# Performance work log

Hardware: AMD Instinct MI355X
Metric: run time of the kernel (lower is better)

The kernel has to match this reference:

```python
import jax, jax.numpy as jnp
import numpy as np

N, E = 50000, 800000
F, H, M = 64, 128, 64  # feature_dim, hidden_dim, message_dim (message_dim must equal feature_dim)


def _mlp(x, W1, b1, W2, b2):
    return jnp.maximum(x @ W1 + b1, 0.0) @ W2 + b2


def setup_inputs() -> dict:
    key = jax.random.key(0)
    ks = jax.random.split(key, 20)
    p = lambda k, s: (jax.random.normal(k, s, jnp.float32) * 0.05)
    return {
        "z_h": jax.random.normal(ks[0], (N, F), jnp.float32),
        "pos_world": jax.random.normal(ks[1], (3,), jnp.float32),
        "edge_index": jax.random.randint(ks[2], (2, E), 0, N),
        "We1": p(ks[3], (2 * F + 8, H)), "be1": p(ks[4], (H,)),
        "We2": p(ks[5], (H, M)), "be2": p(ks[6], (M,)),
        "Wg1": p(ks[7], (2 * F + 8, H)), "bg1": p(ks[8], (H,)),
        "Wg2": p(ks[9], (H, 1)), "bg2": p(ks[10], (1,)),
        "Wn1": p(ks[11], (F + M, H)), "bn1": p(ks[12], (H,)),
        "Wn2": p(ks[13], (H, F)), "bn2": p(ks[14], (F,)),
        "Ww1": p(ks[15], (F + 3, H)), "bw1": p(ks[16], (H,)),
        "Ww2": p(ks[17], (H, M)), "bw2": p(ks[18], (M,)),
    }


def reference(z_h, pos_world, edge_index,
              We1, be1, We2, be2,
              Wg1, bg1, Wg2, bg2,
              Wn1, bn1, Wn2, bn2,
              Ww1, bw1, Ww2, bw2):
    src, tgt = edge_index[0], edge_index[1]
    zs = z_h[src]  # [E, F]
    zt = z_h[tgt]  # [E, F]

    # edge features: diff(3) + dist(1) + vel cross product(3) + its norm(1)
    diff = zs[:, 0:3] - zt[:, 0:3]
    dist = jnp.sum(diff * diff, axis=-1, keepdims=True)
    cross = jnp.cross(zs[:, 3:6], zt[:, 3:6])
    cross_n = jnp.linalg.norm(cross, axis=-1, keepdims=True)
    e_feat = jnp.concatenate([diff, dist, cross, cross_n], axis=-1)  # [E, 8]

    inp_edge = jnp.concatenate([zs, zt, e_feat], axis=-1)  # [E, 2F+8]
    m = _mlp(inp_edge, We1, be1, We2, be2)                 # [E, M]
    w = jax.nn.sigmoid(_mlp(inp_edge, Wg1, bg1, Wg2, bg2))  # [E, 1]

    # scatter_add weighted messages to target nodes
    m_agg_h = jax.ops.segment_sum(w * m, tgt, num_segments=N)  # [N, F] (M == F)

    # world message: sum over all nodes, broadcast back
    diff_world = z_h[:, 0:3] - pos_world
    inp_world = jnp.concatenate([z_h, diff_world], axis=-1)  # [N, F+3]
    m_h_w = _mlp(inp_world, Ww1, bw1, Ww2, bw2)              # [N, M]
    m_agg_w = jnp.sum(m_h_w, axis=0, keepdims=True)          # [1, M] -> broadcast

    m_agg_total = m_agg_h + m_agg_w
    inp_node = jnp.concatenate([z_h, m_agg_total], axis=-1)  # [N, F+M]
    delta_z_h = _mlp(inp_node, Wn1, bn1, Wn2, bn2)           # [N, F]
    return delta_z_h
```

## Files before the change

### kernel.cpp

```cpp
#include <hip/hip_runtime.h>
#include <math.h>

#define NN 50000
#define NE 800000
#define EBLOCKS (NE / 64)
#define WBLOCKS ((NN + 63) / 64)

typedef float     f32x4  __attribute__((ext_vector_type(4)));
typedef __bf16    bf16x8 __attribute__((ext_vector_type(8)));
typedef _Float16  f16x2  __attribute__((ext_vector_type(2)));
typedef _Float16  f16x8  __attribute__((ext_vector_type(8)));

#define WE1F_OFF 0
#define WE2F_OFF 5120
#define WN1F_OFF 6144
#define WN2F_OFF 8192
#define WW1F_OFF 9216
#define WW2F_OFF 10752
#define NCHUNKS  11776


__device__ inline bf16x8 pack8(float4 a, float4 b) {
    bf16x8 r;
    r[0] = (__bf16)a.x; r[1] = (__bf16)a.y; r[2] = (__bf16)a.z; r[3] = (__bf16)a.w;
    r[4] = (__bf16)b.x; r[5] = (__bf16)b.y; r[6] = (__bf16)b.z; r[7] = (__bf16)b.w;
    return r;
}

__device__ inline void pk_atomic_add_f16(void* addr, f16x2 v) {
#if __has_builtin(__builtin_amdgcn_global_atomic_fadd_v2f16)
    __builtin_amdgcn_global_atomic_fadd_v2f16((f16x2*)addr, v);
#else
    asm volatile("global_atomic_pk_add_f16 %0, %1, off"
                 :: "v"(addr), "v"(v) : "memory");
#endif
}

__global__ __launch_bounds__(256) void pack_weights(
    const float* __restrict__ We1, const float* __restrict__ Wg1,
    const float* __restrict__ We2, const float* __restrict__ Wn1,
    const float* __restrict__ Wn2, const float* __restrict__ Ww1,
    const float* __restrict__ Ww2, bf16x8* __restrict__ wsF)
{
    int c = blockIdx.x * 256 + threadIdx.x;
    if (c >= NCHUNKS) return;
    const int lane = c & 63, l16 = lane & 15, row8 = ((lane >> 4) & 3) * 8;
    bf16x8 p;
    if (c < WE2F_OFF) {
        int ct = (c >> 6) & 15, kc = c >> 10;
        int col = ct * 16 + l16;
        const float* src = (col < 128) ? (We1 + col) : (Wg1 + (col - 128));
#pragma unroll
        for (int i = 0; i < 8; i++) {
            int r = kc * 32 + row8 + i;
            p[i] = (__bf16)((r < 136) ? src[(size_t)r * 128] : 0.f);
        }
    } else if (c < WN1F_OFF) {
        int cc = c - WE2F_OFF; int ct = (cc >> 6) & 3, kc = cc >> 8;
        int col = ct * 16 + l16;
#pragma unroll
        for (int i = 0; i < 8; i++)
            p[i] = (__bf16)We2[(size_t)(kc * 32 + row8 + i) * 64 + col];
    } else if (c < WN2F_OFF) {
        int cc = c - WN1F_OFF; int ct = (cc >> 6) & 7, kc = cc >> 9;
        int col = ct * 16 + l16;
#pragma unroll
        for (int i = 0; i < 8; i++)
            p[i] = (__bf16)Wn1[(size_t)(kc * 32 + row8 + i) * 128 + col];
    } else if (c < WW1F_OFF) {
        int cc = c - WN2F_OFF; int ct = (cc >> 6) & 3, kc = cc >> 8;
        int col = ct * 16 + l16;
#pragma unroll
        for (int i = 0; i < 8; i++)
            p[i] = (__bf16)Wn2[(size_t)(kc * 32 + row8 + i) * 64 + col];
    } else if (c < WW2F_OFF) {
        int cc = c - WW1F_OFF; int ct = (cc >> 6) & 7, kc = cc >> 9;
        int col = ct * 16 + l16;
#pragma unroll
        for (int i = 0; i < 8; i++) {
            int r = kc * 32 + row8 + i;
            p[i] = (__bf16)((r < 67) ? Ww1[(size_t)r * 128 + col] : 0.f);
        }
    } else {
        int cc = c - WW2F_OFF; int ct = (cc >> 6) & 3, kc = cc >> 8;
        int col = ct * 16 + l16;
#pragma unroll
        for (int i = 0; i < 8; i++)
            p[i] = (__bf16)Ww2[(size_t)(kc * 32 + row8 + i) * 64 + col];
    }
    wsF[c] = p;
}

union FusedLds {
    bf16x8 XF[1280];
    struct {
        bf16x8   HF[1024];
        _Float16 M[64 * 68];
    } s;
};

__global__ __launch_bounds__(512, 6) void fused_kernel(
    const float* __restrict__ z_h, const int* __restrict__ ei,
    const bf16x8* __restrict__ We1F, const bf16x8* __restrict__ We2F,
    const float* __restrict__ be1, const float* __restrict__ be2,
    const float* __restrict__ bg1, const float* __restrict__ Wg2,
    const float* __restrict__ bg2,
    const float* __restrict__ pos_world,
    const bf16x8* __restrict__ Ww1F, const bf16x8* __restrict__ Ww2F,
    const float* __restrict__ bw1, const float* __restrict__ bw2,
    float* __restrict__ magg_rows,
    float* __restrict__ m_agg_w)
{
    __shared__ FusedLds U;
    __shared__ int   tgt_s[64];
    __shared__ float gred[4][64];
    __shared__ float wgt[64];

    const int t = threadIdx.x;
    const int lane = t & 63, w = t >> 6;
    const int quad = lane >> 4, l16 = lane & 15;

    if (blockIdx.x >= EBLOCKS) {
        const int n0 = (blockIdx.x - EBLOCKS) * 64;
        {
            int nn = t >> 3, q = t & 7;
            int mt = nn >> 4, l16e = nn & 15;
            int node = n0 + nn; if (node >= NN) node = NN - 1;
            if (q < 4) {
                const float4* zr = (const float4*)(z_h + (long)node * 64) + q * 4;
                float4 a0 = zr[0], a1 = zr[1], a2 = zr[2], a3 = zr[3];
                int kcs = q >> 1, qa = (q & 1) * 2;
                U.XF[(kcs * 4 + mt) * 64 + qa * 16 + l16e]       = pack8(a0, a1);
                U.XF[(kcs * 4 + mt) * 64 + (qa + 1) * 16 + l16e] = pack8(a2, a3);
            } else if (q == 4) {
                float4 a0 = *(const float4*)(z_h + (long)node * 64);
                bf16x8 f;
#pragma unroll
                for (int i = 0; i < 8; i++) f[i] = (__bf16)0.f;
                f[0] = (__bf16)(a0.x - pos_world[0]);
                f[1] = (__bf16)(a0.y - pos_world[1]);
                f[2] = (__bf16)(a0.z - pos_world[2]);
                U.XF[(8 + mt) * 64 + l16e] = f;
            } else {
                bf16x8 z;
#pragma unroll
                for (int i = 0; i < 8; i++) z[i] = (__bf16)0.f;
                U.XF[(8 + mt) * 64 + (q - 4) * 16 + l16e] = z;
            }
        }
        __syncthreads();

        f32x4 acc[4];
        {
            float b = bw1[w * 16 + l16];
#pragma unroll
            for (int mt = 0; mt < 4; mt++) { f32x4 v = {b, b, b, b}; acc[mt] = v; }
        }
#pragma unroll
        for (int kc = 0; kc < 3; kc++) {
            bf16x8 bfr = Ww1F[(kc * 8 + w) * 64 + lane];
#pragma unroll
            for (int mt = 0; mt < 4; mt++)
                acc[mt] = __builtin_amdgcn_mfma_f32_16x16x32_bf16(
                    U.XF[(kc * 4 + mt) * 64 + lane], bfr, acc[mt], 0, 0, 0);
        }
        __syncthreads();

        {
            __bf16* HFp = (__bf16*)U.s.HF;
            int cw = w * 16 + l16;
            int kc2 = cw >> 5, quad2 = (cw >> 3) & 3, ii = cw & 7;
#pragma unroll
            for (int mt = 0; mt < 4; mt++)
#pragma unroll
                for (int r = 0; r < 4; r++)
                    HFp[(((kc2 * 4 + mt) * 64) + quad2 * 16 + quad * 4 + r) * 8 + ii] =
                        (__bf16)fmaxf(acc[mt][r], 0.f);
        }
        __syncthreads();

        {
            const int nt = w & 3, mh = w >> 2;
            f32x4 acc2[2];
            float b2 = bw2[nt * 16 + l16];
#pragma unroll
            for (int m = 0; m < 2; m++) { f32x4 v = {b2, b2, b2, b2}; acc2[m] = v; }
#pragma unroll
            for (int kc = 0; kc < 4; kc++) {
                bf16x8 b2f = Ww2F[(kc * 4 + nt) * 64 + lane];
#pragma unroll
                for (int m = 0; m < 2; m++)
                    acc2[m] = __builtin_amdgcn_mfma_f32_16x16x32_bf16(
                        U.s.HF[(kc * 4 + mh * 2 + m) * 64 + lane], b2f, acc2[m], 0, 0, 0);
            }
            float s = 0.f;
#pragma unroll
            for (int m = 0; m < 2; m++)
#pragma unroll
                for (int r = 0; r < 4; r++) {
                    int node = n0 + (mh * 2 + m) * 16 + quad * 4 + r;
                    s += (node < NN) ? acc2[m][r] : 0.f;
                }
            s += __shfl_xor(s, 16, 64);
            s += __shfl_xor(s, 32, 64);
            if (quad == 0) atomicAdd(m_agg_w + nt * 16 + l16, s);
        }
        return;
    }

    const int e0 = blockIdx.x * 64;

    {
        const int ee = t >> 3, q = t & 7;
        const int side = q >> 2, sub = q & 3;
        const int mt = ee >> 4, l16e = ee & 15;
        const int eg = e0 + ee;
        const int row = side ? ei[NE + eg] : ei[eg];
        if (q == 4) tgt_s[ee] = row;
        const float4* zr = (const float4*)(z_h + (long)row * 64) + sub * 4;
        float4 a0 = zr[0], a1 = zr[1], a2 = zr[2], a3 = zr[3];
        const int kcs = (sub >> 1) + side * 2, qa = (sub & 1) * 2;
        U.XF[(kcs * 4 + mt) * 64 + qa * 16 + l16e]       = pack8(a0, a1);
        U.XF[(kcs * 4 + mt) * 64 + (qa + 1) * 16 + l16e] = pack8(a2, a3);
        if (q == 0) {
            const float4* zt = (const float4*)(z_h + (long)ei[NE + eg] * 64);
            float4 t0 = zt[0], t1 = zt[1];
            float dx = a0.x - t0.x, dy = a0.y - t0.y, dz = a0.z - t0.z;
            float ax = a0.w, ay = a1.x, az = a1.y;
            float bx = t0.w, by = t1.x, bz = t1.y;
            float cx = ay * bz - az * by;
            float cy = az * bx - ax * bz;
            float cz = ax * by - ay * bx;
            bf16x8 f;
            f[0] = (__bf16)dx; f[1] = (__bf16)dy; f[2] = (__bf16)dz;
            f[3] = (__bf16)(dx * dx + dy * dy + dz * dz);
            f[4] = (__bf16)cx; f[5] = (__bf16)cy; f[6] = (__bf16)cz;
            f[7] = (__bf16)sqrtf(cx * cx + cy * cy + cz * cz);
            U.XF[(16 + mt) * 64 + l16e] = f;
        } else if (q >= 5) {
            bf16x8 z;
#pragma unroll
            for (int i = 0; i < 8; i++) z[i] = (__bf16)0.f;
            U.XF[(16 + mt) * 64 + (q - 4) * 16 + l16e] = z;
        }
    }
    __syncthreads();

    f32x4 acc[4][2];
#pragma unroll
    for (int nt = 0; nt < 2; nt++) {
        int col = (w * 2 + nt) * 16 + l16;
        float b = (col < 128) ? be1[col] : bg1[col - 128];
#pragma unroll
        for (int mt = 0; mt < 4; mt++) { f32x4 v = {b, b, b, b}; acc[mt][nt] = v; }
    }
    bf16x8 bcur0 = We1F[(w * 2) * 64 + lane];
    bf16x8 bcur1 = We1F[(w * 2 + 1) * 64 + lane];
#pragma unroll
    for (int kc = 0; kc < 5; kc++) {
        bf16x8 bnx0, bnx1;
        if (kc < 4) {
            bnx0 = We1F[((kc + 1) * 16 + w * 2) * 64 + lane];
            bnx1 = We1F[((kc + 1) * 16 + w * 2 + 1) * 64 + lane];
        }
#pragma unroll
        for (int mt = 0; mt < 4; mt++) {
            bf16x8 af = U.XF[(kc * 4 + mt) * 64 + lane];
            acc[mt][0] = __builtin_amdgcn_mfma_f32_16x16x32_bf16(af, bcur0, acc[mt][0], 0, 0, 0);
            acc[mt][1] = __builtin_amdgcn_mfma_f32_16x16x32_bf16(af, bcur1, acc[mt][1], 0, 0, 0);
        }
        bcur0 = bnx0; bcur1 = bnx1;
    }
    __syncthreads();

    if (w < 4) {
        __bf16* HFp = (__bf16*)U.s.HF;
#pragma unroll
        for (int nt = 0; nt < 2; nt++) {
            int cw = (w * 2 + nt) * 16 + l16;
            int kc2 = cw >> 5, quad2 = (cw >> 3) & 3, ii = cw & 7;
#pragma unroll
            for (int mt = 0; mt < 4; mt++)
#pragma unroll
                for (int r = 0; r < 4; r++)
                    HFp[(((kc2 * 4 + mt) * 64) + quad2 * 16 + quad * 4 + r) * 8 + ii] =
                        (__bf16)fmaxf(acc[mt][nt][r], 0.f);
        }
    } else {
        float gp[4][4];
#pragma unroll
        for (int mt = 0; mt < 4; mt++)
#pragma unroll
            for (int r = 0; r < 4; r++) gp[mt][r] = 0.f;
#pragma unroll
        for (int nt = 0; nt < 2; nt++) {
            float wg = Wg2[((w - 4) * 2 + nt) * 16 + l16];
#pragma unroll
            for (int mt = 0; mt < 4; mt++)
#pragma unroll
                for (int r = 0; r < 4; r++)
                    gp[mt][r] += fmaxf(acc[mt][nt][r], 0.f) * wg;
        }
#pragma unroll
        for (int mask = 1; mask < 16; mask <<= 1)
#pragma unroll
            for (int mt = 0; mt < 4; mt++)
#pragma unroll
                for (int r = 0; r < 4; r++)
                    gp[mt][r] += __shfl_xor(gp[mt][r], mask, 64);
        if (l16 == 0) {
#pragma unroll
            for (int mt = 0; mt < 4; mt++)
#pragma unroll
                for (int r = 0; r < 4; r++)
                    gred[(w - 4) & 3][mt * 16 + quad * 4 + r] = gp[mt][r];
        }
    }
    __syncthreads();

    if (t < 64) {
        float g = bg2[0] + gred[0][t] + gred[1][t] + gred[2][t] + gred[3][t];
        wgt[t] = 1.f / (1.f + __expf(-g));
    }

    f32x4 acc2[4];
    if (w < 4) {
        float b2 = be2[w * 16 + l16];
#pragma unroll
        for (int mt = 0; mt < 4; mt++) { f32x4 v = {b2, b2, b2, b2}; acc2[mt] = v; }
        bf16x8 c2 = We2F[w * 64 + lane];
#pragma unroll
        for (int kc = 0; kc < 4; kc++) {
            bf16x8 n2;
            if (kc < 3) n2 = We2F[((kc + 1) * 4 + w) * 64 + lane];
#pragma unroll
            for (int mt = 0; mt < 4; mt++)
                acc2[mt] = __builtin_amdgcn_mfma_f32_16x16x32_bf16(
                    U.s.HF[(kc * 4 + mt) * 64 + lane], c2, acc2[mt], 0, 0, 0);
            c2 = n2;
        }
    }
    __syncthreads();

    if (w < 4) {
#pragma unroll
        for (int mt = 0; mt < 4; mt++)
#pragma unroll
            for (int r = 0; r < 4; r++) {
                int edge = mt * 16 + quad * 4 + r;
                U.s.M[edge * 68 + w * 16 + l16] =
                    (_Float16)(acc2[mt][r] * wgt[edge]);
            }
    }
    __syncthreads();

    {
        const int p = t & 31, eb = t >> 5;
        char* base = (char*)magg_rows;
#pragma unroll
        for (int k = 0; k < 4; k++) {
            int e = eb + k * 16;
            f16x2 v = *(const f16x2*)&U.s.M[e * 68 + p * 2];
            pk_atomic_add_f16(base + (long)tgt_s[e] * 256 + p * 4, v);
        }
    }
}

__global__ __launch_bounds__(512, 4) void node_kernel(
    const float* __restrict__ z_h,
    const float* __restrict__ m_agg_w,
    const bf16x8* __restrict__ Wn1F, const bf16x8* __restrict__ Wn2F,
    const float* __restrict__ bn1, const float* __restrict__ bn2,
    float* __restrict__ outp)
{
    __shared__ union { bf16x8 XF[1024]; bf16x8 HF[1024]; } U;
    const int t = threadIdx.x;
    const int n0 = blockIdx.x * 64;
    const int lane = t & 63, w = t >> 6;
    const int quad = lane >> 4, l16 = lane & 15;

    {
        int nn = t >> 3, q = t & 7;
        int mt = nn >> 4, l16e = nn & 15;
        int node = n0 + nn; if (node >= NN) node = NN - 1;
        int half = q >> 2, sub = q & 3;
        bf16x8 c0, c1;
        if (half == 0) {
            const float4* zr = (const float4*)(z_h + (long)node * 64) + sub * 4;
            c0 = pack8(zr[0], zr[1]);
            c1 = pack8(zr[2], zr[3]);
        } else {
            const f16x8* mr = (const f16x8*)((const char*)outp + (long)node * 256) + sub * 2;
            f16x8 r0 = mr[0], r1 = mr[1];
            const float* mw = m_agg_w + sub * 16;
#pragma unroll
            for (int i = 0; i < 8; i++) {
                c0[i] = (__bf16)((float)r0[i] + mw[i]);
                c1[i] = (__bf16)((float)r1[i] + mw[i + 8]);
            }
        }
        int kcs = (sub >> 1) + half * 2, qa = (sub & 1) * 2;
        U.XF[(kcs * 4 + mt) * 64 + qa * 16 + l16e]       = c0;
        U.XF[(kcs * 4 + mt) * 64 + (qa + 1) * 16 + l16e] = c1;
    }
    __syncthreads();

    f32x4 acc[4];
    {
        float b = bn1[w * 16 + l16];
#pragma unroll
        for (int mt = 0; mt < 4; mt++) { f32x4 v = {b, b, b, b}; acc[mt] = v; }
    }
#pragma unroll
    for (int kc = 0; kc < 4; kc++) {
        bf16x8 bfr = Wn1F[(kc * 8 + w) * 64 + lane];
#pragma unroll
        for (int mt = 0; mt < 4; mt++)
            acc[mt] = __builtin_amdgcn_mfma_f32_16x16x32_bf16(
                U.XF[(kc * 4 + mt) * 64 + lane], bfr, acc[mt], 0, 0, 0);
    }
    __syncthreads();

    {
        __bf16* HFp = (__bf16*)U.HF;
        int cw = w * 16 + l16;
        int kc2 = cw >> 5, quad2 = (cw >> 3) & 3, ii = cw & 7;
#pragma unroll
        for (int mt = 0; mt < 4; mt++)
#pragma unroll
            for (int r = 0; r < 4; r++)
                HFp[(((kc2 * 4 + mt) * 64) + quad2 * 16 + quad * 4 + r) * 8 + ii] =
                    (__bf16)fmaxf(acc[mt][r], 0.f);
    }
    __syncthreads();

    {
        const int nt = w & 3, mh = w >> 2;
        f32x4 acc2[2];
        float b2 = bn2[nt * 16 + l16];
#pragma unroll
        for (int m = 0; m < 2; m++) { f32x4 v = {b2, b2, b2, b2}; acc2[m] = v; }
#pragma unroll
        for (int kc = 0; kc < 4; kc++) {
            bf16x8 b2f = Wn2F[(kc * 4 + nt) * 64 + lane];
#pragma unroll
            for (int m = 0; m < 2; m++)
                acc2[m] = __builtin_amdgcn_mfma_f32_16x16x32_bf16(
                    U.HF[(kc * 4 + mh * 2 + m) * 64 + lane], b2f, acc2[m], 0, 0, 0);
        }
#pragma unroll
        for (int m = 0; m < 2; m++)
#pragma unroll
            for (int r = 0; r < 4; r++) {
                int node = n0 + (mh * 2 + m) * 16 + quad * 4 + r;
                if (node < NN)
                    outp[(long)node * 64 + nt * 16 + l16] = acc2[m][r];
            }
    }
}

extern "C" void kernel_launch(void* const* d_in, const int* in_sizes, int n_in,
                              void* d_out, int out_size, void* d_ws, size_t ws_size,
                              hipStream_t stream)
{
    const float* z_h       = (const float*)d_in[0];
    const float* pos_world = (const float*)d_in[1];
    const int*   ei        = (const int*)d_in[2];
    const float* We1 = (const float*)d_in[3];  const float* be1 = (const float*)d_in[4];
    const float* We2 = (const float*)d_in[5];  const float* be2 = (const float*)d_in[6];
    const float* Wg1 = (const float*)d_in[7];  const float* bg1 = (const float*)d_in[8];
    const float* Wg2 = (const float*)d_in[9];  const float* bg2 = (const float*)d_in[10];
    const float* Wn1 = (const float*)d_in[11]; const float* bn1 = (const float*)d_in[12];
    const float* Wn2 = (const float*)d_in[13]; const float* bn2 = (const float*)d_in[14];
    const float* Ww1 = (const float*)d_in[15]; const float* bw1 = (const float*)d_in[16];
    const float* Ww2 = (const float*)d_in[17]; const float* bw2 = (const float*)d_in[18];

    float*  outp    = (float*)d_out;
    float*  m_agg_w = (float*)d_ws;
    bf16x8* wsF     = (bf16x8*)((char*)d_ws + 256);

    hipMemsetAsync(d_out, 0, (size_t)NN * 64 * sizeof(float), stream);
    hipMemsetAsync(d_ws, 0, 256, stream);

    pack_weights<<<(NCHUNKS + 255) / 256, 256, 0, stream>>>(
        We1, Wg1, We2, Wn1, Wn2, Ww1, Ww2, wsF);
    fused_kernel<<<EBLOCKS + WBLOCKS, 512, 0, stream>>>(
        z_h, ei, wsF + WE1F_OFF, wsF + WE2F_OFF,
        be1, be2, bg1, Wg2, bg2,
        pos_world, wsF + WW1F_OFF, wsF + WW2F_OFF, bw1, bw2,
        outp, m_agg_w);
    node_kernel<<<(NN + 63) / 64, 512, 0, stream>>>(
        z_h, m_agg_w, wsF + WN1F_OFF, wsF + WN2F_OFF, bn1, bn2, outp);
}
```

Measured before the change: 295.7 us.

## Process 128 edges per block in fused edge kernel

Doubles the edge tile from 64 to 128 edges per block, so each wave's weight fragments loaded from global memory are reused across twice as many MFMA row tiles. The gather is reorganized so each thread loads both the source and target rows for one quarter of an edge, which also removes the separate target reload used for edge features. This doubles the accumulator register and LDS footprint, and the launch bound drops from 6 to 4 blocks per CU, which may reduce occupancy and latency hiding for the gather-heavy loads. The world-message blocks share the kernel and now run with the same larger LDS allocation.

Result: no change. 296.8 us (+0.4%).

```diff
diff --git a/kernel.cpp b/kernel.cpp
--- a/kernel.cpp
+++ b/kernel.cpp
@@ -3,7 +3,8 @@
 
 #define NN 50000
 #define NE 800000
-#define EBLOCKS (NE / 64)
+#define EB 128
+#define EBLOCKS (NE / EB)
 #define WBLOCKS ((NN + 63) / 64)
 
 typedef float     f32x4  __attribute__((ext_vector_type(4)));
@@ -92,14 +93,14 @@
 }
 
 union FusedLds {
-    bf16x8 XF[1280];
+    bf16x8 XF[2560];
     struct {
-        bf16x8   HF[1024];
-        _Float16 M[64 * 68];
+        bf16x8   HF[2048];
+        _Float16 M[EB * 68];
     } s;
 };
 
-__global__ __launch_bounds__(512, 6) void fused_kernel(
+__global__ __launch_bounds__(512, 4) void fused_kernel(
     const float* __restrict__ z_h, const int* __restrict__ ei,
     const bf16x8* __restrict__ We1F, const bf16x8* __restrict__ We2F,
     const float* __restrict__ be1, const float* __restrict__ be2,
@@ -112,9 +113,9 @@
     float* __restrict__ m_agg_w)
 {
     __shared__ FusedLds U;
-    __shared__ int   tgt_s[64];
-    __shared__ float gred[4][64];
-    __shared__ float wgt[64];
+    __shared__ int   tgt_s[EB];
+    __shared__ float gred[4][EB];
+    __shared__ float wgt[EB];
 
     const int t = threadIdx.x;
     const int lane = t & 63, w = t >> 6;
@@ -208,26 +209,28 @@
         return;
     }
 
-    const int e0 = blockIdx.x * 64;
-
-    {
-        const int ee = t >> 3, q = t & 7;
-        const int side = q >> 2, sub = q & 3;
+    const int e0 = blockIdx.x * EB;
+
+    {
+        const int ee = t >> 2, sub = t & 3;
         const int mt = ee >> 4, l16e = ee & 15;
         const int eg = e0 + ee;
-        const int row = side ? ei[NE + eg] : ei[eg];
-        if (q == 4) tgt_s[ee] = row;
-        const float4* zr = (const float4*)(z_h + (long)row * 64) + sub * 4;
-        float4 a0 = zr[0], a1 = zr[1], a2 = zr[2], a3 = zr[3];
-        const int kcs = (sub >> 1) + side * 2, qa = (sub & 1) * 2;
-        U.XF[(kcs * 4 + mt) * 64 + qa * 16 + l16e]       = pack8(a0, a1);
-        U.XF[(kcs * 4 + mt) * 64 + (qa + 1) * 16 + l16e] = pack8(a2, a3);
-        if (q == 0) {
-            const float4* zt = (const float4*)(z_h + (long)ei[NE + eg] * 64);
-            float4 t0 = zt[0], t1 = zt[1];
-            float dx = a0.x - t0.x, dy = a0.y - t0.y, dz = a0.z - t0.z;
+        const int rs = ei[eg], rt = ei[NE + eg];
+        if (sub == 0) tgt_s[ee] = rt;
+        const int qa = (sub & 1) * 2;
+        const float4* zs = (const float4*)(z_h + (long)rs * 64) + sub * 4;
+        float4 a0 = zs[0], a1 = zs[1], a2 = zs[2], a3 = zs[3];
+        const float4* zt = (const float4*)(z_h + (long)rt * 64) + sub * 4;
+        float4 b0 = zt[0], b1 = zt[1], b2 = zt[2], b3 = zt[3];
+        const int kcs = (sub >> 1);
+        U.XF[(kcs * 8 + mt) * 64 + qa * 16 + l16e]             = pack8(a0, a1);
+        U.XF[(kcs * 8 + mt) * 64 + (qa + 1) * 16 + l16e]       = pack8(a2, a3);
+        U.XF[((kcs + 2) * 8 + mt) * 64 + qa * 16 + l16e]       = pack8(b0, b1);
+        U.XF[((kcs + 2) * 8 + mt) * 64 + (qa + 1) * 16 + l16e] = pack8(b2, b3);
+        if (sub == 0) {
+            float dx = a0.x - b0.x, dy = a0.y - b0.y, dz = a0.z - b0.z;
             float ax = a0.w, ay = a1.x, az = a1.y;
-            float bx = t0.w, by = t1.x, bz = t1.y;
+            float bx = b0.w, by = b1.x, bz = b1.y;
             float cx = ay * bz - az * by;
             float cy = az * bx - ax * bz;
             float cz = ax * by - ay * bx;
@@ -236,23 +239,23 @@
             f[3] = (__bf16)(dx * dx + dy * dy + dz * dz);
             f[4] = (__bf16)cx; f[5] = (__bf16)cy; f[6] = (__bf16)cz;
             f[7] = (__bf16)sqrtf(cx * cx + cy * cy + cz * cz);
-            U.XF[(16 + mt) * 64 + l16e] = f;
-        } else if (q >= 5) {
+            U.XF[(32 + mt) * 64 + l16e] = f;
+        } else {
             bf16x8 z;
 #pragma unroll
             for (int i = 0; i < 8; i++) z[i] = (__bf16)0.f;
-            U.XF[(16 + mt) * 64 + (q - 4) * 16 + l16e] = z;
-        }
-    }
-    __syncthreads();
-
-    f32x4 acc[4][2];
+            U.XF[(32 + mt) * 64 + sub * 16 + l16e] = z;
+        }
+    }
+    __syncthreads();
+
+    f32x4 acc[8][2];
 #pragma unroll
     for (int nt = 0; nt < 2; nt++) {
         int col = (w * 2 + nt) * 16 + l16;
         float b = (col < 128) ? be1[col] : bg1[col - 128];
 #pragma unroll
-        for (int mt = 0; mt < 4; mt++) { f32x4 v = {b, b, b, b}; acc[mt][nt] = v; }
+        for (int mt = 0; mt < 8; mt++) { f32x4 v = {b, b, b, b}; acc[mt][nt] = v; }
     }
     bf16x8 bcur0 = We1F[(w * 2) * 64 + lane];
     bf16x8 bcur1 = We1F[(w * 2 + 1) * 64 + lane];
@@ -264,8 +267,8 @@
             bnx1 = We1F[((kc + 1) * 16 + w * 2 + 1) * 64 + lane];
         }
 #pragma unroll
-        for (int mt = 0; mt < 4; mt++) {
-            bf16x8 af = U.XF[(kc * 4 + mt) * 64 + lane];
+        for (int mt = 0; mt < 8; mt++) {
+            bf16x8 af = U.XF[(kc * 8 + mt) * 64 + lane];
             acc[mt][0] = __builtin_amdgcn_mfma_f32_16x16x32_bf16(af, bcur0, acc[mt][0], 0, 0, 0);
             acc[mt][1] = __builtin_amdgcn_mfma_f32_16x16x32_bf16(af, bcur1, acc[mt][1], 0, 0, 0);
         }
@@ -280,23 +283,23 @@
             int cw = (w * 2 + nt) * 16 + l16;
             int kc2 = cw >> 5, quad2 = (cw >> 3) & 3, ii = cw & 7;
 #pragma unroll
-            for (int mt = 0; mt < 4; mt++)
+            for (int mt = 0; mt < 8; mt++)
 #pragma unroll
                 for (int r = 0; r < 4; r++)
-                    HFp[(((kc2 * 4 + mt) * 64) + quad2 * 16 + quad * 4 + r) * 8 + ii] =
+                    HFp[(((kc2 * 8 + mt) * 64) + quad2 * 16 + quad * 4 + r) * 8 + ii] =
                         (__bf16)fmaxf(acc[mt][nt][r], 0.f);
         }
     } else {
-        float gp[4][4];
-#pragma unroll
-        for (int mt = 0; mt < 4; mt++)
+        float gp[8][4];
+#pragma unroll
+        for (int mt = 0; mt < 8; mt++)
 #pragma unroll
             for (int r = 0; r < 4; r++) gp[mt][r] = 0.f;
 #pragma unroll
         for (int nt = 0; nt < 2; nt++) {
             float wg = Wg2[((w - 4) * 2 + nt) * 16 + l16];
 #pragma unroll
-            for (int mt = 0; mt < 4; mt++)
+            for (int mt = 0; mt < 8; mt++)
 #pragma unroll
                 for (int r = 0; r < 4; r++)
                     gp[mt][r] += fmaxf(acc[mt][nt][r], 0.f) * wg;
@@ -304,39 +307,39 @@
 #pragma unroll
         for (int mask = 1; mask < 16; mask <<= 1)
 #pragma unroll
-            for (int mt = 0; mt < 4; mt++)
+            for (int mt = 0; mt < 8; mt++)
 #pragma unroll
                 for (int r = 0; r < 4; r++)
                     gp[mt][r] += __shfl_xor(gp[mt][r], mask, 64);
         if (l16 == 0) {
 #pragma unroll
-            for (int mt = 0; mt < 4; mt++)
+            for (int mt = 0; mt < 8; mt++)
 #pragma unroll
                 for (int r = 0; r < 4; r++)
-                    gred[(w - 4) & 3][mt * 16 + quad * 4 + r] = gp[mt][r];
-        }
-    }
-    __syncthreads();
-
-    if (t < 64) {
+                    gred[w - 4][mt * 16 + quad * 4 + r] = gp[mt][r];
+        }
+    }
+    __syncthreads();
+
+    if (t < EB) {
         float g = bg2[0] + gred[0][t] + gred[1][t] + gred[2][t] + gred[3][t];
         wgt[t] = 1.f / (1.f + __expf(-g));
     }
 
-    f32x4 acc2[4];
+    f32x4 acc2[8];
     if (w < 4) {
         float b2 = be2[w * 16 + l16];
 #pragma unroll
-        for (int mt = 0; mt < 4; mt++) { f32x4 v = {b2, b2, b2, b2}; acc2[mt] = v; }
+        for (int mt = 0; mt < 8; mt++) { f32x4 v = {b2, b2, b2, b2}; acc2[mt] = v; }
         bf16x8 c2 = We2F[w * 64 + lane];
 #pragma unroll
         for (int kc = 0; kc < 4; kc++) {
             bf16x8 n2;
             if (kc < 3) n2 = We2F[((kc + 1) * 4 + w) * 64 + lane];
 #pragma unroll
-            for (int mt = 0; mt < 4; mt++)
+            for (int mt = 0; mt < 8; mt++)
                 acc2[mt] = __builtin_amdgcn_mfma_f32_16x16x32_bf16(
-                    U.s.HF[(kc * 4 + mt) * 64 + lane], c2, acc2[mt], 0, 0, 0);
+                    U.s.HF[(kc * 8 + mt) * 64 + lane], c2, acc2[mt], 0, 0, 0);
             c2 = n2;
         }
     }
@@ -344,7 +347,7 @@
 
     if (w < 4) {
 #pragma unroll
-        for (int mt = 0; mt < 4; mt++)
+        for (int mt = 0; mt < 8; mt++)
 #pragma unroll
             for (int r = 0; r < 4; r++) {
                 int edge = mt * 16 + quad * 4 + r;
@@ -358,7 +361,7 @@
         const int p = t & 31, eb = t >> 5;
         char* base = (char*)magg_rows;
 #pragma unroll
-        for (int k = 0; k < 4; k++) {
+        for (int k = 0; k < 8; k++) {
             int e = eb + k * 16;
             f16x2 v = *(const f16x2*)&U.s.M[e * 68 + p * 2];
             pk_atomic_add_f16(base + (long)tgt_s[e] * 256 + p * 4, v);
```

## Pre-convert node features to bf16 in output buffer for halved gather traffic

Applied to the files above, without the earlier changes.

A new prep kernel converts z_h to bf16 once per node and stores it in the unused upper half of each output row, next to the fp16 aggregation slots. The edge kernel then gathers 128-byte bf16 rows for source and target instead of 256-byte fp32 rows, and computes the edge geometry features from the bf16 values. The node kernel reads the same bf16 copy. This halves the random-gather bandwidth over 800k edges at the cost of one extra small kernel, and the geometric features now come from bf16-rounded positions, which lowers their precision.

Measured after the change: 294.4 us. Within noise of the previous version (-0.5%).

```diff
diff --git a/kernel.cpp b/kernel.cpp
--- a/kernel.cpp
+++ b/kernel.cpp
@@ -34,6 +34,17 @@
     asm volatile("global_atomic_pk_add_f16 %0, %1, off"
                  :: "v"(addr), "v"(v) : "memory");
 #endif
+}
+
+__global__ __launch_bounds__(512) void prep_z(
+    const float* __restrict__ z, float* __restrict__ db)
+{
+    int i = blockIdx.x * 512 + threadIdx.x;
+    if (i >= NN * 8) return;
+    int node = i >> 3, c = i & 7;
+    const float4* s = (const float4*)(z + (long)node * 64) + c * 2;
+    float4 a = s[0], b = s[1];
+    *(bf16x8*)((char*)db + (long)node * 256 + 128 + c * 16) = pack8(a, b);
 }
 
 __global__ __launch_bounds__(256) void pack_weights(
@@ -212,22 +223,23 @@
 
     {
         const int ee = t >> 3, q = t & 7;
-        const int side = q >> 2, sub = q & 3;
         const int mt = ee >> 4, l16e = ee & 15;
         const int eg = e0 + ee;
-        const int row = side ? ei[NE + eg] : ei[eg];
-        if (q == 4) tgt_s[ee] = row;
-        const float4* zr = (const float4*)(z_h + (long)row * 64) + sub * 4;
-        float4 a0 = zr[0], a1 = zr[1], a2 = zr[2], a3 = zr[3];
-        const int kcs = (sub >> 1) + side * 2, qa = (sub & 1) * 2;
-        U.XF[(kcs * 4 + mt) * 64 + qa * 16 + l16e]       = pack8(a0, a1);
-        U.XF[(kcs * 4 + mt) * 64 + (qa + 1) * 16 + l16e] = pack8(a2, a3);
+        const int rs = ei[eg], rt = ei[NE + eg];
+        const bf16x8* zs = (const bf16x8*)((const char*)magg_rows + (long)rs * 256 + 128);
+        const bf16x8* zt = (const bf16x8*)((const char*)magg_rows + (long)rt * 256 + 128);
+        bf16x8 sa = zs[q];
+        bf16x8 ta = zt[q];
+        const int kcs = q >> 2, qslot = q & 3;
+        U.XF[(kcs * 4 + mt) * 64 + qslot * 16 + l16e]       = sa;
+        U.XF[((kcs + 2) * 4 + mt) * 64 + qslot * 16 + l16e] = ta;
+        if (q == 4) tgt_s[ee] = rt;
         if (q == 0) {
-            const float4* zt = (const float4*)(z_h + (long)ei[NE + eg] * 64);
-            float4 t0 = zt[0], t1 = zt[1];
-            float dx = a0.x - t0.x, dy = a0.y - t0.y, dz = a0.z - t0.z;
-            float ax = a0.w, ay = a1.x, az = a1.y;
-            float bx = t0.w, by = t1.x, bz = t1.y;
+            float dx = (float)sa[0] - (float)ta[0];
+            float dy = (float)sa[1] - (float)ta[1];
+            float dz = (float)sa[2] - (float)ta[2];
+            float ax = (float)sa[3], ay = (float)sa[4], az = (float)sa[5];
+            float bx = (float)ta[3], by = (float)ta[4], bz = (float)ta[5];
             float cx = ay * bz - az * by;
             float cy = az * bx - ax * bz;
             float cz = ax * by - ay * bx;
@@ -367,7 +379,6 @@
 }
 
 __global__ __launch_bounds__(512, 4) void node_kernel(
-    const float* __restrict__ z_h,
     const float* __restrict__ m_agg_w,
     const bf16x8* __restrict__ Wn1F, const bf16x8* __restrict__ Wn2F,
     const float* __restrict__ bn1, const float* __restrict__ bn2,
@@ -386,9 +397,8 @@
         int half = q >> 2, sub = q & 3;
         bf16x8 c0, c1;
         if (half == 0) {
-            const float4* zr = (const float4*)(z_h + (long)node * 64) + sub * 4;
-            c0 = pack8(zr[0], zr[1]);
-            c1 = pack8(zr[2], zr[3]);
+            const bf16x8* zr = (const bf16x8*)((const char*)outp + (long)node * 256 + 128) + sub * 2;
+            c0 = zr[0]; c1 = zr[1];
         } else {
             const f16x8* mr = (const f16x8*)((const char*)outp + (long)node * 256) + sub * 2;
             f16x8 r0 = mr[0], r1 = mr[1];
@@ -482,6 +492,7 @@
     hipMemsetAsync(d_out, 0, (size_t)NN * 64 * sizeof(float), stream);
     hipMemsetAsync(d_ws, 0, 256, stream);
 
+    prep_z<<<(NN * 8 + 511) / 512, 512, 0, stream>>>(z_h, outp);
     pack_weights<<<(NCHUNKS + 255) / 256, 256, 0, stream>>>(
         We1, Wg1, We2, Wn1, Wn2, Ww1, Ww2, wsF);
     fused_kernel<<<EBLOCKS + WBLOCKS, 512, 0, stream>>>(
@@ -490,5 +501,5 @@
         pos_world, wsF + WW1F_OFF, wsF + WW2F_OFF, bw1, bw2,
         outp, m_agg_w);
     node_kernel<<<(NN + 63) / 64, 512, 0, stream>>>(
-        z_h, m_agg_w, wsF + WN1F_OFF, wsF + WN2F_OFF, bn1, bn2, outp);
-}
+        m_agg_w, wsF + WN1F_OFF, wsF + WN2F_OFF, bn1, bn2, outp);
+}
```
